# Kernel optimization log

Hardware: AMD Instinct MI355X
Metric: run time of the kernel (lower is better)

## Reference

```python
import jax, jax.numpy as jnp
import numpy as np

B, C, T, H, W = 1024, 1, 500, 7, 7
HID, OUT = 16, 2


def setup_inputs() -> dict:
    key = jax.random.key(0)
    k1, k2, k3, k4 = jax.random.split(key, 4)
    rppg_embeddings = jax.random.normal(k1, (B, C, T, H, W), dtype=jnp.float32)
    rBr = jax.random.normal(k2, (B, C, T), dtype=jnp.float32)
    # final_dense_layer params: Linear(500,16) -> Dropout (identity at eval) -> Linear(16,2)
    W1 = jax.random.normal(k3, (C * T, HID), dtype=jnp.float32) / np.sqrt(C * T)
    b1 = jnp.zeros((HID,), dtype=jnp.float32)
    W2 = jax.random.normal(k4, (HID, OUT), dtype=jnp.float32) / np.sqrt(HID)
    b2 = jnp.zeros((OUT,), dtype=jnp.float32)
    return {"rppg_embeddings": rppg_embeddings, "rBr": rBr,
            "W1": W1, "b1": b1, "W2": W2, "b2": b2}


def reference(rppg_embeddings, rBr, W1, b1, W2, b2):
    # AvgPool3d(kernel=[1,7,7], stride=1, pad=0) on (B,C,T,7,7) -> (B,C,T,1,1):
    # equivalent to mean over the full 7x7 spatial window.
    x = jnp.mean(rppg_embeddings, axis=(-2, -1))            # (B, C, T)
    # batched FFT phase along time (replaces the per-(b,c) Python loop)
    phase = jnp.angle(jnp.fft.fft(x, axis=-1))              # (B, C, T)
    flat = phase.reshape(phase.shape[0], -1)                # (B, C*T) = (B, 500)
    h = flat @ W1 + b1                                      # (B, 16); dropout = identity (eval)
    rBP = h @ W2 + b2                                       # (B, 2)
    return rBP
```

## Files before the change

### kernel.cpp

```cpp
#include <hip/hip_runtime.h>
#include <math.h>

#ifndef M_PI
#define M_PI 3.14159265358979323846
#endif

#define T_LEN 500
#define HW49  49
#define HID   16
#define NOUT  2

__global__ __launch_bounds__(256) void pool_kernel(
    const float* __restrict__ rppg, float* __restrict__ xout)
{
    const int n   = blockIdx.x * 256 + threadIdx.x;
    const int row = n / 125;
    const int g   = n - row * 125;
    const float4* g4 = (const float4*)rppg + (size_t)row * 6125 + g * 49;

    float acc[4] = {0.f, 0.f, 0.f, 0.f};
    #pragma unroll
    for (int j = 0; j < 49; ++j) {
        const float4 v = g4[j];
        acc[(4 * j + 0) / 49] += v.x;
        acc[(4 * j + 1) / 49] += v.y;
        acc[(4 * j + 2) / 49] += v.z;
        acc[(4 * j + 3) / 49] += v.w;
    }
    float4 o;
    o.x = acc[0] * (1.0f / 49.0f);
    o.y = acc[1] * (1.0f / 49.0f);
    o.z = acc[2] * (1.0f / 49.0f);
    o.w = acc[3] * (1.0f / 49.0f);
    *(float4*)(xout + (size_t)row * T_LEN + g * 4) = o;
}

__global__ __launch_bounds__(256, 4) void dft_head_kernel(
    const float* __restrict__ xin,
    const float* __restrict__ W1,
    const float* __restrict__ b1,
    const float* __restrict__ W2,
    const float* __restrict__ b2,
    float* __restrict__ out)
{
    __shared__ __align__(16) float xsh[512];
    __shared__ float wsum[4][HID + 1];
    const int tid = threadIdx.x;
    const int row = blockIdx.x;

    {
        float4* x4s = (float4*)xsh;
        const float4* xr4 = (const float4*)(xin + (size_t)row * T_LEN);
        if (tid < 125) x4s[tid] = xr4[tid];
        else if (tid < 128) x4s[tid] = float4{0.f, 0.f, 0.f, 0.f};
    }
    __syncthreads();

    float hp[HID];
    #pragma unroll
    for (int j = 0; j < HID; ++j) hp[j] = 0.f;

    if (tid <= 249) {
        const int k = tid;
        const double ang = (double)k * (-2.0 * M_PI / 500.0);
        double c1, s1;
        sincos(ang, &s1, &c1);
        const double c2 = fma(c1, c1, -(s1 * s1));
        const double s2 = 2.0 * c1 * s1;
        const float c1f = (float)c1, s1f = (float)s1;
        const float c2f = (float)c2, s2f = (float)s2;
        const float c3f = (float)fma(c1, c2, -(s1 * s2));
        const float s3f = (float)fma(c1, s2,  (s1 * c2));
        const float c4f = (float)fma(c2, c2, -(s2 * s2));
        const float s4f = (float)(2.0 * c2 * s2);

        float cw = 1.f, sw = 0.f;
        float re0 = 0.f, im0 = 0.f, re1 = 0.f, im1 = 0.f;
        float re2 = 0.f, im2 = 0.f, re3 = 0.f, im3 = 0.f;
        const float4* x4 = (const float4*)xsh;
        float4 xv = x4[0];
        for (int j = 0; j < 125; ++j) {
            const float4 nx = x4[j + 1];
            re0 = fmaf(xv.x, cw, re0); im0 = fmaf(xv.x, sw, im0);
            re1 = fmaf(xv.y, cw, re1); im1 = fmaf(xv.y, sw, im1);
            re2 = fmaf(xv.z, cw, re2); im2 = fmaf(xv.z, sw, im2);
            re3 = fmaf(xv.w, cw, re3); im3 = fmaf(xv.w, sw, im3);
            const float tc = fmaf(cw, c4f, -(sw * s4f));
            sw = fmaf(cw, s4f, sw * c4f);
            cw = tc;
            xv = nx;
        }
        const float re = re0 + fmaf(c1f, re1, -(s1f * im1))
                             + fmaf(c2f, re2, -(s2f * im2))
                             + fmaf(c3f, re3, -(s3f * im3));
        const float im = im0 + fmaf(c1f, im1,  (s1f * re1))
                             + fmaf(c2f, im2,  (s2f * re2))
                             + fmaf(c3f, im3,  (s3f * re3));
        const float ph = atan2f(im, re);

        if (k == 0) {
            const float* w = W1;
            #pragma unroll
            for (int j = 0; j < HID; ++j) hp[j] = ph * w[j];
        } else {
            const float* wa = W1 + k * HID;
            const float* wb = W1 + (T_LEN - k) * HID;
            #pragma unroll
            for (int j = 0; j < HID; ++j) hp[j] = ph * (wa[j] - wb[j]);
        }
    }

    #pragma unroll
    for (int j = 0; j < HID; ++j) {
        float v = hp[j];
        v += __shfl_xor(v, 1);  v += __shfl_xor(v, 2);
        v += __shfl_xor(v, 4);  v += __shfl_xor(v, 8);
        v += __shfl_xor(v, 16); v += __shfl_xor(v, 32);
        hp[j] = v;
    }
    if ((tid & 63) == 0) {
        const int w = tid >> 6;
        #pragma unroll
        for (int j = 0; j < HID; ++j) wsum[w][j] = hp[j];
    }
    __syncthreads();

    if (tid < NOUT) {
        const int o = tid;
        float acc = b2[o];
        #pragma unroll
        for (int j = 0; j < HID; ++j) {
            const float h = wsum[0][j] + wsum[1][j] + wsum[2][j] + wsum[3][j] + b1[j];
            acc = fmaf(h, W2[j * NOUT + o], acc);
        }
        out[row * NOUT + o] = acc;
    }
}

__global__ __launch_bounds__(256, 4) void bp_fused2_kernel(
    const float* __restrict__ rppg,
    const float* __restrict__ W1, const float* __restrict__ b1,
    const float* __restrict__ W2, const float* __restrict__ b2,
    float* __restrict__ out)
{
    __shared__ __align__(16) float stage[2][3136];
    __shared__ __align__(16) float xsh[512];
    __shared__ float wsum[4][HID + 1];
    const int tid = threadIdx.x;
    const int row = blockIdx.x;
    const float4* src4 = (const float4*)(rppg + (size_t)row * (T_LEN * HW49));

    if (tid < 12) xsh[T_LEN + tid] = 0.f;
    const float4 fz = {0.f, 0.f, 0.f, 0.f};
    float4 r0, r1, r2, r3;
    r0 = src4[tid]; r1 = src4[tid + 256]; r2 = src4[tid + 512];
    r3 = (tid < 16) ? src4[tid + 768] : fz;
    {
        float4* st = (float4*)stage[0];
        st[tid] = r0; st[tid + 256] = r1; st[tid + 512] = r2;
        if (tid < 16) st[tid + 768] = r3;
    }
    __syncthreads();
    const int bin  = tid >> 2;
    const int part = tid & 3;
    const int nels = (part < 3) ? 13 : 10;
    const int boff = bin * HW49 + part * 13;
    for (int c = 0; c < 8; ++c) {
        if (c < 7) {
            const int n4 = (c + 1 < 7) ? 784 : 637;
            const float4* b4 = src4 + 784 * (c + 1);
            r0 = (tid       < n4) ? b4[tid      ] : fz;
            r1 = (tid + 256 < n4) ? b4[tid + 256] : fz;
            r2 = (tid + 512 < n4) ? b4[tid + 512] : fz;
            r3 = (tid + 768 < n4) ? b4[tid + 768] : fz;
        }
        const int bins_c = (c < 7) ? 64 : 52;
        {
            const float* bufp = stage[c & 1];
            float s = 0.f;
            if (bin < bins_c) {
                const float* p = bufp + boff;
                for (int j = 0; j < nels; ++j) s += p[j];
            }
            s += __shfl_xor(s, 1);
            s += __shfl_xor(s, 2);
            if (part == 0 && bin < bins_c) xsh[c * 64 + bin] = s * (1.0f / 49.0f);
        }
        __syncthreads();
        if (c < 7) {
            const int n4 = (c + 1 < 7) ? 784 : 637;
            float4* st = (float4*)stage[(c + 1) & 1];
            if (tid       < n4) st[tid      ] = r0;
            if (tid + 256 < n4) st[tid + 256] = r1;
            if (tid + 512 < n4) st[tid + 512] = r2;
            if (tid + 768 < n4) st[tid + 768] = r3;
            __syncthreads();
        }
    }

    float hp[HID];
    #pragma unroll
    for (int j = 0; j < HID; ++j) hp[j] = 0.f;
    if (tid <= 249) {
        const int k = tid;
        const double ang = (double)k * (-2.0 * M_PI / 500.0);
        double c1, s1;
        sincos(ang, &s1, &c1);
        const double c2 = fma(c1, c1, -(s1 * s1));
        const double s2 = 2.0 * c1 * s1;
        const float c1f = (float)c1, s1f = (float)s1;
        const float c2f = (float)c2, s2f = (float)s2;
        const float c3f = (float)fma(c1, c2, -(s1 * s2));
        const float s3f = (float)fma(c1, s2,  (s1 * c2));
        const float c4f = (float)fma(c2, c2, -(s2 * s2));
        const float s4f = (float)(2.0 * c2 * s2);
        float cw = 1.f, sw = 0.f;
        float re0 = 0.f, im0 = 0.f, re1 = 0.f, im1 = 0.f;
        float re2 = 0.f, im2 = 0.f, re3 = 0.f, im3 = 0.f;
        const float4* x4 = (const float4*)xsh;
        float4 xv = x4[0];
        for (int j = 0; j < 125; ++j) {
            const float4 nx = x4[j + 1];
            re0 = fmaf(xv.x, cw, re0); im0 = fmaf(xv.x, sw, im0);
            re1 = fmaf(xv.y, cw, re1); im1 = fmaf(xv.y, sw, im1);
            re2 = fmaf(xv.z, cw, re2); im2 = fmaf(xv.z, sw, im2);
            re3 = fmaf(xv.w, cw, re3); im3 = fmaf(xv.w, sw, im3);
            const float tc = fmaf(cw, c4f, -(sw * s4f));
            sw = fmaf(cw, s4f, sw * c4f);
            cw = tc;
            xv = nx;
        }
        const float re = re0 + fmaf(c1f, re1, -(s1f * im1))
                             + fmaf(c2f, re2, -(s2f * im2))
                             + fmaf(c3f, re3, -(s3f * im3));
        const float im = im0 + fmaf(c1f, im1,  (s1f * re1))
                             + fmaf(c2f, im2,  (s2f * re2))
                             + fmaf(c3f, im3,  (s3f * re3));
        const float ph = atan2f(im, re);
        if (k == 0) {
            const float* w = W1;
            #pragma unroll
            for (int j = 0; j < HID; ++j) hp[j] = ph * w[j];
        } else {
            const float* wa = W1 + k * HID;
            const float* wb = W1 + (T_LEN - k) * HID;
            #pragma unroll
            for (int j = 0; j < HID; ++j) hp[j] = ph * (wa[j] - wb[j]);
        }
    }
    #pragma unroll
    for (int j = 0; j < HID; ++j) {
        float v = hp[j];
        v += __shfl_xor(v, 1);  v += __shfl_xor(v, 2);
        v += __shfl_xor(v, 4);  v += __shfl_xor(v, 8);
        v += __shfl_xor(v, 16); v += __shfl_xor(v, 32);
        hp[j] = v;
    }
    if ((tid & 63) == 0) {
        const int w = tid >> 6;
        #pragma unroll
        for (int j = 0; j < HID; ++j) wsum[w][j] = hp[j];
    }
    __syncthreads();
    if (tid < NOUT) {
        const int o = tid;
        float acc = b2[o];
        #pragma unroll
        for (int j = 0; j < HID; ++j) {
            const float h = wsum[0][j] + wsum[1][j] + wsum[2][j] + wsum[3][j] + b1[j];
            acc = fmaf(h, W2[j * NOUT + o], acc);
        }
        out[row * NOUT + o] = acc;
    }
}

extern "C" void kernel_launch(void* const* d_in, const int* in_sizes, int n_in,
                              void* d_out, int out_size, void* d_ws, size_t ws_size,
                              hipStream_t stream) {
    const float* rppg = (const float*)d_in[0];
    const float* W1 = (const float*)d_in[2];
    const float* b1 = (const float*)d_in[3];
    const float* W2 = (const float*)d_in[4];
    const float* b2 = (const float*)d_in[5];
    float* out = (float*)d_out;

    const size_t need = (size_t)1024 * T_LEN * sizeof(float);
    if (ws_size >= need) {
        float* x = (float*)d_ws;
        pool_kernel<<<dim3(500), dim3(256), 0, stream>>>(rppg, x);
        dft_head_kernel<<<dim3(1024), dim3(256), 0, stream>>>(x, W1, b1, W2, b2, out);
    } else {
        bp_fused2_kernel<<<dim3(1024), dim3(256), 0, stream>>>(rppg, W1, b1, W2, b2, out);
    }
}
```

Baseline: 186.9 us.

## Stage pooling input through LDS with coalesced float4 loads per half-row

```diff
diff --git a/kernel.cpp b/kernel.cpp
--- a/kernel.cpp
+++ b/kernel.cpp
@@ -13,26 +13,29 @@
 __global__ __launch_bounds__(256) void pool_kernel(
     const float* __restrict__ rppg, float* __restrict__ xout)
 {
-    const int n   = blockIdx.x * 256 + threadIdx.x;
-    const int row = n / 125;
-    const int g   = n - row * 125;
-    const float4* g4 = (const float4*)rppg + (size_t)row * 6125 + g * 49;
-
-    float acc[4] = {0.f, 0.f, 0.f, 0.f};
-    #pragma unroll
-    for (int j = 0; j < 49; ++j) {
-        const float4 v = g4[j];
-        acc[(4 * j + 0) / 49] += v.x;
-        acc[(4 * j + 1) / 49] += v.y;
-        acc[(4 * j + 2) / 49] += v.z;
-        acc[(4 * j + 3) / 49] += v.w;
-    }
-    float4 o;
-    o.x = acc[0] * (1.0f / 49.0f);
-    o.y = acc[1] * (1.0f / 49.0f);
-    o.z = acc[2] * (1.0f / 49.0f);
-    o.w = acc[3] * (1.0f / 49.0f);
-    *(float4*)(xout + (size_t)row * T_LEN + g * 4) = o;
+    __shared__ __align__(16) float lds[12348];
+    const int tid  = threadIdx.x;
+    const int row  = blockIdx.x >> 1;
+    const int half = blockIdx.x & 1;
+    const int bin0 = half ? 252 : 0;
+    const int nbin = half ? 248 : 252;
+    const int nf4  = half ? 3038 : 3087;
+    const float4* src = (const float4*)(rppg + (size_t)row * (T_LEN * HW49)
+                                        + bin0 * HW49);
+    float4* dst = (float4*)lds;
+    #pragma unroll
+    for (int s = 0; s < 13; ++s) {
+        const int i = tid + 256 * s;
+        if (i < nf4) dst[i] = src[i];
+    }
+    __syncthreads();
+    if (tid < nbin) {
+        const float* p = lds + tid * HW49;
+        float acc = 0.f;
+        #pragma unroll
+        for (int j = 0; j < HW49; ++j) acc += p[j];
+        xout[(size_t)row * T_LEN + bin0 + tid] = acc * (1.0f / 49.0f);
+    }
 }
 
 __global__ __launch_bounds__(256, 4) void dft_head_kernel(
@@ -287,7 +290,7 @@
     const size_t need = (size_t)1024 * T_LEN * sizeof(float);
     if (ws_size >= need) {
         float* x = (float*)d_ws;
-        pool_kernel<<<dim3(500), dim3(256), 0, stream>>>(rppg, x);
+        pool_kernel<<<dim3(2048), dim3(256), 0, stream>>>(rppg, x);
         dft_head_kernel<<<dim3(1024), dim3(256), 0, stream>>>(x, W1, b1, W2, b2, out);
     } else {
         bp_fused2_kernel<<<dim3(1024), dim3(256), 0, stream>>>(rppg, W1, b1, W2, b2, out);
```

Measured after the change: 169.8 us. 9.2% less time.
